# Kernel tuning notes

Hardware: AMD Instinct MI355X
Metric: run time of the kernel (lower is better)

Reference implementation:

```python
import jax, jax.numpy as jnp
import numpy as np

B, M, D, L = 16384, 16, 128, 26  # words, word length, feature dim, num labels


def setup_inputs() -> dict:
    key = jax.random.key(0)
    k1, k2, k3, k4 = jax.random.split(key, 4)
    X = jax.random.normal(k1, (B, M, D), dtype=jnp.float32)
    Y = jax.random.randint(k2, (B, M), 0, L, dtype=jnp.int64)
    W = jax.random.normal(k3, (L, D), dtype=jnp.float32) * 0.1
    T = jax.random.normal(k4, (L, L), dtype=jnp.float32) * 0.1
    return {"X": X, "Y": Y, "W": W, "T": T}


def reference(X, Y, W, T):
    # Negative conditional log-likelihood of a linear-chain CRF (get_crf_obj).
    # emissions: e[b, s, k] = <W[k], X[b, s]>
    emit = jnp.einsum('bsd,kd->bsk', X, W)  # [B, M, L]
    bsz = X.shape[0]

    # forward recurrence: alpha[i, j] = logsumexp_k(emit[i-1, k] + T[k, j] + alpha[i-1, k])
    def step(alpha, e_prev):
        # alpha, e_prev: [B, L]; T: [L(k), L(j)]
        new = jax.nn.logsumexp(alpha[:, :, None] + e_prev[:, :, None] + T[None, :, :], axis=1)
        return new, None

    alpha0 = jnp.zeros((bsz, emit.shape[-1]), dtype=emit.dtype)
    # scan over positions 0..M-2 (emissions at the previous step)
    alpha_last, _ = jax.lax.scan(step, alpha0, jnp.moveaxis(emit[:, :-1, :], 1, 0))

    # log partition: logsumexp_k(emit[M-1, k] + alpha[M-1, k])
    log_z = jax.nn.logsumexp(emit[:, -1, :] + alpha_last, axis=-1)  # [B]

    # node potential: sum_s emit[s, Y[s]]
    node = jnp.take_along_axis(emit, Y[:, :, None], axis=2)[:, :, 0].sum(axis=1)  # [B]
    # edge potential: sum_s T[Y[s], Y[s+1]]
    edge = T[Y[:, :-1], Y[:, 1:]].sum(axis=1)  # [B]

    log_likelihood = jnp.sum(node + edge - log_z)
    return -log_likelihood
```

## Files before the change

kernel.cpp:

```cpp
#include <hip/hip_runtime.h>
#include <math.h>


#define B_TOT 16384
#define M_LEN 16
#define D_DIM 128
#define L_LAB 26
#define WPB 4
#define NBLOCKS (B_TOT / WPB)
#define LOG2E 1.4426950408889634f
#define LN2   0.6931471805599453f

typedef short v8s __attribute__((ext_vector_type(8)));
typedef float v4f __attribute__((ext_vector_type(4)));

static __device__ __forceinline__ unsigned bf16u(float f) {
    unsigned u = __float_as_uint(f);
    u += 0x7fff + ((u >> 16) & 1);
    return u >> 16;
}
static __device__ __forceinline__ unsigned pkbf(float lo, float hi) {
    return bf16u(lo) | (bf16u(hi) << 16);
}
static __device__ __forceinline__ float fexp2(float x) {
#if __has_builtin(__builtin_amdgcn_exp2f)
    return __builtin_amdgcn_exp2f(x);
#else
    return exp2f(x);
#endif
}
static __device__ __forceinline__ float flog2(float x) {
#if __has_builtin(__builtin_amdgcn_logf)
    return __builtin_amdgcn_logf(x);
#else
    return log2f(x);
#endif
}

__global__ void prep_kernel(const float* __restrict__ W, uint4* __restrict__ wsW) {
    const int l = threadIdx.x;
    const int c16 = l & 15, quad = l >> 4;
    #pragma unroll
    for (int f = 0; f < 8; ++f) {
        const int tile = f >> 2, kk = f & 3;
        const int label = tile * 16 + c16;
        const int base = kk * 32 + quad * 8;
        unsigned d[4];
        #pragma unroll
        for (int p = 0; p < 4; ++p) {
            float a = 0.f, bb = 0.f;
            if (label < L_LAB) {
                a  = W[label * D_DIM + base + 2 * p]     * LOG2E;
                bb = W[label * D_DIM + base + 2 * p + 1] * LOG2E;
            }
            d[p] = pkbf(a, bb);
        }
        wsW[l * 8 + f] = make_uint4(d[0], d[1], d[2], d[3]);
    }
}

__global__ __launch_bounds__(256, 4) void crf_kernel(
    const float* __restrict__ X, const int* __restrict__ Y,
    const float* __restrict__ T, const uint4* __restrict__ wsW,
    float* __restrict__ out)
{
    const int lane = threadIdx.x & 63;
    const int wave = threadIdx.x >> 6;
    const int k2 = lane >> 1;
    const int h  = lane & 1;
    const int jj = (k2 < L_LAB) ? k2 : 0;
    const int c16 = lane & 15;
    const int quad = lane >> 4;

    __shared__ float Ts[L_LAB * L_LAB];
    __shared__ float Es[WPB][M_LEN * 32];
    __shared__ float red[WPB];

    for (int i = threadIdx.x; i < L_LAB * L_LAB; i += 256) Ts[i] = T[i];

    uint4 wf[8];
    #pragma unroll
    for (int f = 0; f < 8; ++f) wf[f] = wsW[lane * 8 + f];

    float Tr2[13];
    #pragma unroll
    for (int u = 0; u < 13; ++u) Tr2[u] = T[(h * 13 + u) * L_LAB + jj] * LOG2E;

    __syncthreads();

    const int b = blockIdx.x * WPB + wave;
    const float* xb = X + (size_t)b * (M_LEN * D_DIM);

    v4f acc0 = {0.f, 0.f, 0.f, 0.f};
    v4f acc1 = {0.f, 0.f, 0.f, 0.f};
    #pragma unroll
    for (int kk = 0; kk < 4; ++kk) {
        const float4* xp = (const float4*)(xb + c16 * D_DIM + kk * 32 + quad * 8);
        float4 xa = xp[0];
        float4 xc = xp[1];
        uint4 au = make_uint4(pkbf(xa.x, xa.y), pkbf(xa.z, xa.w),
                              pkbf(xc.x, xc.y), pkbf(xc.z, xc.w));
        v8s af = *(v8s*)&au;
        v8s b0 = *(v8s*)&wf[kk];
        v8s b1 = *(v8s*)&wf[4 + kk];
        acc0 = __builtin_amdgcn_mfma_f32_16x16x32_bf16(af, b0, acc0, 0, 0, 0);
        acc1 = __builtin_amdgcn_mfma_f32_16x16x32_bf16(af, b1, acc1, 0, 0, 0);
    }
    #pragma unroll
    for (int r = 0; r < 4; ++r) {
        const int s = quad * 4 + r;
        Es[wave][s * 32 + c16] = acc0[r];
        Es[wave][s * 32 + 16 + c16] = acc1[r];
    }

    float ne = 0.f;
    if (lane < M_LEN) {
        const int ys = Y[(size_t)b * M_LEN + lane];
        ne = Es[wave][lane * 32 + ys] * LN2;
        if (lane < M_LEN - 1) {
            const int yn = Y[(size_t)b * M_LEN + lane + 1];
            ne += Ts[ys * L_LAB + yn];
        }
    }
    #pragma unroll
    for (int off = 32; off >= 1; off >>= 1) ne += __shfl_xor(ne, off);

    float alpha = 0.f, offs = 0.f;
    const int baddr = 104 * h;
    for (int s = 0; s < M_LEN - 1; ++s) {
        const float c = __shfl(alpha, 0);
        const float ae = alpha - c + Es[wave][s * 32 + jj];
        const int aei = __float_as_int(ae);
        float s0 = 0.f, s1 = 0.f;
        #pragma unroll
        for (int u = 0; u < 12; u += 2) {
            float t0 = __int_as_float(__builtin_amdgcn_ds_bpermute(baddr + 8 * u, aei)) + Tr2[u];
            float t1 = __int_as_float(__builtin_amdgcn_ds_bpermute(baddr + 8 * u + 8, aei)) + Tr2[u + 1];
            s0 += fexp2(t0);
            s1 += fexp2(t1);
        }
        s0 += fexp2(__int_as_float(__builtin_amdgcn_ds_bpermute(baddr + 96, aei)) + Tr2[12]);
        float ss = s0 + s1;
        ss += __shfl_xor(ss, 1);
        alpha = flog2(ss);
        offs += c;
    }

    const float fin = (h == 0 && k2 < L_LAB) ? (alpha + Es[wave][(M_LEN - 1) * 32 + k2]) : 0.f;
    float ez = (h == 0 && k2 < L_LAB) ? fexp2(fin) : 0.f;
    #pragma unroll
    for (int off = 32; off >= 1; off >>= 1) ez += __shfl_xor(ez, off);
    const float logz = (flog2(ez) + offs) * LN2;

    const float local = logz - ne;
    if (lane == 0) red[wave] = local;
    __syncthreads();
    if (threadIdx.x == 0) atomicAdd(out, (red[0] + red[1]) + (red[2] + red[3]));
}

extern "C" void kernel_launch(void* const* d_in, const int* in_sizes, int n_in,
                              void* d_out, int out_size, void* d_ws, size_t ws_size,
                              hipStream_t stream) {
    const float* X = (const float*)d_in[0];
    const int*   Y = (const int*)d_in[1];
    const float* W = (const float*)d_in[2];
    const float* T = (const float*)d_in[3];
    float* out = (float*)d_out;
    uint4* wsW = (uint4*)d_ws;

    hipMemsetAsync(out, 0, sizeof(float), stream);
    prep_kernel<<<1, 64, 0, stream>>>(W, wsW);
    crf_kernel<<<NBLOCKS, 256, 0, stream>>>(X, Y, T, wsW, out);
}
```

Measured before the change: 232.0 us.

## Run CRF forward recurrence in linear (exp) space with two words per wave

Replaces the log-space logsumexp recurrence, which used per-step exp2, log2 and ds_bpermute, with a linear-space matrix-vector product. Emissions are exponentiated once, and the transition matrix is precomputed as exp(T) scaled by a fixed per-step offset (DELTA). Each wave now handles two words in its two 32-lane halves, which halves the block count, and alpha is exchanged through LDS rows. The catch is possible overflow or underflow, since it relies on a fixed rescaling constant instead of a per-step max subtraction.

```diff
diff --git a/kernel.cpp b/kernel.cpp
--- a/kernel.cpp
+++ b/kernel.cpp
@@ -7,9 +7,11 @@
 #define D_DIM 128
 #define L_LAB 26
 #define WPB 4
-#define NBLOCKS (B_TOT / WPB)
+#define NBLOCKS (B_TOT / (WPB * 2))
 #define LOG2E 1.4426950408889634f
 #define LN2   0.6931471805599453f
+#define DELTA 5.7f
+#define ESTR 36
 
 typedef short v8s __attribute__((ext_vector_type(8)));
 typedef float v4f __attribute__((ext_vector_type(4)));
@@ -37,7 +39,8 @@
 #endif
 }
 
-__global__ void prep_kernel(const float* __restrict__ W, uint4* __restrict__ wsW) {
+__global__ void prep_kernel(const float* __restrict__ W, const float* __restrict__ T,
+                            uint4* __restrict__ wsW, float* __restrict__ wsP) {
     const int l = threadIdx.x;
     const int c16 = l & 15, quad = l >> 4;
     #pragma unroll
@@ -57,23 +60,28 @@
         }
         wsW[l * 8 + f] = make_uint4(d[0], d[1], d[2], d[3]);
     }
+    for (int i = l; i < 1024; i += 64) {
+        const int j = i >> 5, k = i & 31;
+        wsP[i] = (j < L_LAB && k < L_LAB)
+               ? exp2f(T[k * L_LAB + j] * LOG2E - DELTA) : 0.f;
+    }
 }
 
 __global__ __launch_bounds__(256, 4) void crf_kernel(
     const float* __restrict__ X, const int* __restrict__ Y,
     const float* __restrict__ T, const uint4* __restrict__ wsW,
-    float* __restrict__ out)
+    const float* __restrict__ wsP, float* __restrict__ out)
 {
     const int lane = threadIdx.x & 63;
     const int wave = threadIdx.x >> 6;
-    const int k2 = lane >> 1;
-    const int h  = lane & 1;
-    const int jj = (k2 < L_LAB) ? k2 : 0;
+    const int g = lane >> 5;
+    const int j = lane & 31;
     const int c16 = lane & 15;
     const int quad = lane >> 4;
 
     __shared__ float Ts[L_LAB * L_LAB];
-    __shared__ float Es[WPB][M_LEN * 32];
+    __shared__ float Ee[WPB][2][M_LEN * ESTR];
+    __shared__ float vrow[WPB][2][ESTR];
     __shared__ float red[WPB];
 
     for (int i = threadIdx.x; i < L_LAB * L_LAB; i += 256) Ts[i] = T[i];
@@ -81,79 +89,93 @@
     uint4 wf[8];
     #pragma unroll
     for (int f = 0; f < 8; ++f) wf[f] = wsW[lane * 8 + f];
-
-    float Tr2[13];
-    #pragma unroll
-    for (int u = 0; u < 13; ++u) Tr2[u] = T[(h * 13 + u) * L_LAB + jj] * LOG2E;
+    float Pc[26];
+    {
+        const float* pp = wsP + j * 32;
+        #pragma unroll
+        for (int k = 0; k < 26; ++k) Pc[k] = pp[k];
+    }
 
     __syncthreads();
 
-    const int b = blockIdx.x * WPB + wave;
-    const float* xb = X + (size_t)b * (M_LEN * D_DIM);
+    const int wgid = blockIdx.x * WPB + wave;
 
-    v4f acc0 = {0.f, 0.f, 0.f, 0.f};
-    v4f acc1 = {0.f, 0.f, 0.f, 0.f};
     #pragma unroll
-    for (int kk = 0; kk < 4; ++kk) {
-        const float4* xp = (const float4*)(xb + c16 * D_DIM + kk * 32 + quad * 8);
-        float4 xa = xp[0];
-        float4 xc = xp[1];
-        uint4 au = make_uint4(pkbf(xa.x, xa.y), pkbf(xa.z, xa.w),
-                              pkbf(xc.x, xc.y), pkbf(xc.z, xc.w));
-        v8s af = *(v8s*)&au;
-        v8s b0 = *(v8s*)&wf[kk];
-        v8s b1 = *(v8s*)&wf[4 + kk];
-        acc0 = __builtin_amdgcn_mfma_f32_16x16x32_bf16(af, b0, acc0, 0, 0, 0);
-        acc1 = __builtin_amdgcn_mfma_f32_16x16x32_bf16(af, b1, acc1, 0, 0, 0);
-    }
-    #pragma unroll
-    for (int r = 0; r < 4; ++r) {
-        const int s = quad * 4 + r;
-        Es[wave][s * 32 + c16] = acc0[r];
-        Es[wave][s * 32 + 16 + c16] = acc1[r];
+    for (int g2 = 0; g2 < 2; ++g2) {
+        const float* xb = X + (size_t)(wgid * 2 + g2) * (M_LEN * D_DIM);
+        v4f acc0 = {0.f, 0.f, 0.f, 0.f};
+        v4f acc1 = {0.f, 0.f, 0.f, 0.f};
+        #pragma unroll
+        for (int kk = 0; kk < 4; ++kk) {
+            const float4* xp = (const float4*)(xb + c16 * D_DIM + kk * 32 + quad * 8);
+            float4 xa = xp[0];
+            float4 xc = xp[1];
+            uint4 au = make_uint4(pkbf(xa.x, xa.y), pkbf(xa.z, xa.w),
+                                  pkbf(xc.x, xc.y), pkbf(xc.z, xc.w));
+            v8s af = *(v8s*)&au;
+            v8s b0 = *(v8s*)&wf[kk];
+            v8s b1 = *(v8s*)&wf[4 + kk];
+            acc0 = __builtin_amdgcn_mfma_f32_16x16x32_bf16(af, b0, acc0, 0, 0, 0);
+            acc1 = __builtin_amdgcn_mfma_f32_16x16x32_bf16(af, b1, acc1, 0, 0, 0);
+        }
+        #pragma unroll
+        for (int r = 0; r < 4; ++r) {
+            const int s = quad * 4 + r;
+            Ee[wave][g2][s * ESTR + c16]      = fexp2(acc0[r]);
+            Ee[wave][g2][s * ESTR + 16 + c16] = fexp2(acc1[r]);
+        }
     }
 
     float ne = 0.f;
-    if (lane < M_LEN) {
-        const int ys = Y[(size_t)b * M_LEN + lane];
-        ne = Es[wave][lane * 32 + ys] * LN2;
-        if (lane < M_LEN - 1) {
-            const int yn = Y[(size_t)b * M_LEN + lane + 1];
+    if (j < M_LEN) {
+        const int bb = wgid * 2 + g;
+        const int ys = Y[bb * M_LEN + j];
+        ne = flog2(Ee[wave][g][j * ESTR + ys]) * LN2;
+        if (j < M_LEN - 1) {
+            const int yn = Y[bb * M_LEN + j + 1];
             ne += Ts[ys * L_LAB + yn];
         }
     }
-    #pragma unroll
-    for (int off = 32; off >= 1; off >>= 1) ne += __shfl_xor(ne, off);
+    ne += __shfl_xor(ne, 8);
+    ne += __shfl_xor(ne, 4);
+    ne += __shfl_xor(ne, 2);
+    ne += __shfl_xor(ne, 1);
 
-    float alpha = 0.f, offs = 0.f;
-    const int baddr = 104 * h;
-    for (int s = 0; s < M_LEN - 1; ++s) {
-        const float c = __shfl(alpha, 0);
-        const float ae = alpha - c + Es[wave][s * 32 + jj];
-        const int aei = __float_as_int(ae);
-        float s0 = 0.f, s1 = 0.f;
+    float v[26];
+    {
+        const float* er = &Ee[wave][g][0];
         #pragma unroll
-        for (int u = 0; u < 12; u += 2) {
-            float t0 = __int_as_float(__builtin_amdgcn_ds_bpermute(baddr + 8 * u, aei)) + Tr2[u];
-            float t1 = __int_as_float(__builtin_amdgcn_ds_bpermute(baddr + 8 * u + 8, aei)) + Tr2[u + 1];
-            s0 += fexp2(t0);
-            s1 += fexp2(t1);
+        for (int k = 0; k < 26; ++k) v[k] = er[k];
+    }
+    for (int s = 1; s < M_LEN; ++s) {
+        const float Ej = Ee[wave][g][s * ESTR + j];
+        float u0 = 0.f, u1 = 0.f, u2 = 0.f, u3 = 0.f;
+        #pragma unroll
+        for (int k = 0; k < 24; k += 4) {
+            u0 = fmaf(v[k],     Pc[k],     u0);
+            u1 = fmaf(v[k + 1], Pc[k + 1], u1);
+            u2 = fmaf(v[k + 2], Pc[k + 2], u2);
+            u3 = fmaf(v[k + 3], Pc[k + 3], u3);
         }
-        s0 += fexp2(__int_as_float(__builtin_amdgcn_ds_bpermute(baddr + 96, aei)) + Tr2[12]);
-        float ss = s0 + s1;
-        ss += __shfl_xor(ss, 1);
-        alpha = flog2(ss);
-        offs += c;
+        u0 = fmaf(v[24], Pc[24], u0);
+        u1 = fmaf(v[25], Pc[25], u1);
+        vrow[wave][g][j] = ((u0 + u2) + (u1 + u3)) * Ej;
+        const float* vr = &vrow[wave][g][0];
+        #pragma unroll
+        for (int k = 0; k < 26; ++k) v[k] = vr[k];
     }
 
-    const float fin = (h == 0 && k2 < L_LAB) ? (alpha + Es[wave][(M_LEN - 1) * 32 + k2]) : 0.f;
-    float ez = (h == 0 && k2 < L_LAB) ? fexp2(fin) : 0.f;
+    float s0 = 0.f, s1 = 0.f, s2 = 0.f, s3 = 0.f;
     #pragma unroll
-    for (int off = 32; off >= 1; off >>= 1) ez += __shfl_xor(ez, off);
-    const float logz = (flog2(ez) + offs) * LN2;
+    for (int k = 0; k < 24; k += 4) {
+        s0 += v[k]; s1 += v[k + 1]; s2 += v[k + 2]; s3 += v[k + 3];
+    }
+    s0 += v[24]; s1 += v[25];
+    const float logz = (flog2((s0 + s2) + (s1 + s3)) + 15.f * DELTA) * LN2;
 
-    const float local = logz - ne;
-    if (lane == 0) red[wave] = local;
+    float local = logz - ne;
+    const float other = __shfl(local, 32);
+    if (lane == 0) red[wave] = local + other;
     __syncthreads();
     if (threadIdx.x == 0) atomicAdd(out, (red[0] + red[1]) + (red[2] + red[3]));
 }
@@ -167,8 +189,9 @@
     const float* T = (const float*)d_in[3];
     float* out = (float*)d_out;
     uint4* wsW = (uint4*)d_ws;
+    float* wsP = (float*)((char*)d_ws + 8192);
 
     hipMemsetAsync(out, 0, sizeof(float), stream);
-    prep_kernel<<<1, 64, 0, stream>>>(W, wsW);
-    crf_kernel<<<NBLOCKS, 256, 0, stream>>>(X, Y, T, wsW, out);
+    prep_kernel<<<1, 64, 0, stream>>>(W, T, wsW, wsP);
+    crf_kernel<<<NBLOCKS, 256, 0, stream>>>(X, Y, T, wsW, wsP, out);
 }
```

Measured after the change: 215.8 us. 1.08x faster.
